# Optimization experiments

Measured on AMD Instinct MI355X. Metric: run time of the kernel, lower is better.

## Reference

```python
import jax, jax.numpy as jnp
import numpy as np

B, N, L = 32, 50, 16384  # batch, n_templates, segment length
KT = 4096                # template kernel length


def conv1d(x, w, pad, groups=1):
    # x: [B, Cin, L], w: [Cout, Cin/groups, K] (torch layout)
    return jax.lax.conv_general_dilated(
        x, w, window_strides=(1,), padding=[(pad, pad)],
        dimension_numbers=('NCH', 'OIH', 'NCH'), feature_group_count=groups)


def maxpool3(x):
    # MaxPool1d(kernel=3, stride=3), floor mode (VALID)
    return jax.lax.reduce_window(x, -jnp.inf, jax.lax.max,
                                 (1, 1, 3), (1, 1, 3), 'VALID')


def pad_to(x, m):
    p = (-x.shape[-1]) % m
    pads = ((0, 0),) * (x.ndim - 1) + ((0, p),)
    return jnp.pad(x, pads)


def setup_inputs() -> dict:
    key = jax.random.key(0)
    ks = jax.random.split(key, 12)
    return dict(
        xi=jax.random.normal(ks[0], (B, 2, L), jnp.float32),
        S_t_m12=jax.random.normal(ks[1], (2, 1, L), jnp.float32) * 0.01,
        template=jax.random.normal(ks[2], (N, 2, KT), jnp.float32) * 0.01,
        hh_sqrt=jax.random.uniform(ks[3], (N, 2), jnp.float32) + 0.5,
        W1=jax.random.normal(ks[4], (16, 2, 3), jnp.float32) * 0.1,
        b1=jnp.zeros((16,), jnp.float32),
        W2=jax.random.normal(ks[5], (32, 16, 3), jnp.float32) * 0.1,
        b2=jnp.zeros((32,), jnp.float32),
        W3=jax.random.normal(ks[6], (32, 128), jnp.float32) * 0.1,
        b3=jnp.zeros((32,), jnp.float32),
        W4=jax.random.normal(ks[7], (2, 32), jnp.float32) * 0.1,
        b4=jnp.zeros((2,), jnp.float32),
    )


def reference(xi, S_t_m12, template, hh_sqrt, W1, b1, W2, b2, W3, b3, W4, b4):
    # Whitening matched filter: grouped conv with kernel length L
    y = conv1d(xi, S_t_m12, L - 1, groups=2)          # [B, 2, 2L-1]
    y = pad_to(y, L)                                   # [B, 2, 2L]
    # wrap-fold each channel: reshape(B,2,L).sum over the fold axis
    d_SA = y[:, 0].reshape(-1, 2, L).sum(1)[:, None, :]  # [B,1,L]
    d_SE = y[:, 1].reshape(-1, 2, L).sum(1)[:, None, :]
    h_SA = template[:, 0, :].reshape(-1, 1, KT)          # [N,1,KT]
    h_SE = template[:, 1, :].reshape(-1, 1, KT)
    dh_A = pad_to(conv1d(d_SA, h_SA, KT - 1), L).reshape(-1, N, 2, L).sum(2)  # [B,N,L]
    dh_E = pad_to(conv1d(d_SE, h_SE, KT - 1), L).reshape(-1, N, 2, L).sum(2)
    z = jnp.stack((dh_A, dh_E), -1).transpose(0, 2, 1, 3)  # [B,L,N,2]
    z = z / hh_sqrt                                         # broadcast [N,2]
    z = z.max(axis=1).transpose(0, 2, 1)                    # [B,2,N]
    # small CNN + MLP head
    h = maxpool3(jax.nn.sigmoid(conv1d(z, W1, 0) + b1[None, :, None]))  # [B,16,16]
    h = maxpool3(jax.nn.sigmoid(conv1d(h, W2, 0) + b2[None, :, None]))  # [B,32,4]
    h = h.reshape(h.shape[0], -1)                                        # [B,128]
    h = jax.nn.relu(h @ W3.T + b3)
    return h @ W4.T + b4                                                 # [B,2]
```

## Files before the change

kernel.cpp:

```cpp
#include <hip/hip_runtime.h>
#include <math.h>

#define L_LEN 16384
#define M_LEN 8192
#define KT_LEN 4096
#define BB 32
#define NTPL 50
#define SPEC_STRIDE 8224
#define NSIG 166
#define NT 512
#define PI_F 3.14159265358979323846f

typedef float cf2 __attribute__((ext_vector_type(2)));

__device__ __forceinline__ cf2 cmul(cf2 a, cf2 b) {
    cf2 byx = __builtin_shufflevector(b, b, 1, 0);
    return (cf2){a.x, a.x} * b + (cf2){-a.y, a.y} * byx;
}
__device__ __forceinline__ cf2 cmulc(cf2 a, cf2 b) {
    return a * (cf2){b.x, b.x} + (cf2){a.y, -a.x} * (cf2){b.y, b.y};
}
template<int SIGN>
__device__ __forceinline__ cf2 rot90(cf2 z) {
    return (SIGN < 0) ? (cf2){z.y, -z.x} : (cf2){-z.y, z.x};
}
template<int SIGN>
__device__ __forceinline__ cf2 ldT(const cf2* __restrict__ T, int idx) {
    cf2 t = T[idx];
    if (SIGN > 0) t.y = -t.y;
    return t;
}

__device__ __forceinline__ int swz(int i) { return i ^ (((i >> 5) & 15) << 1); }

__device__ __forceinline__ int pos(int f) {
    return ((f & 15) << 9) | (((f >> 4) & 15) << 5) |
           (((f >> 8) & 15) << 1) | ((f >> 12) & 1);
}

template<int SIGN>
__device__ __forceinline__ void dft16(cf2 x[16]) {
    const float S = (SIGN < 0) ? -1.f : 1.f;
    const cf2 w1 = {0.9238795325112867f, S * 0.3826834323650898f};
    const cf2 w2 = {0.7071067811865476f, S * 0.7071067811865476f};
    const cf2 w3 = {0.3826834323650898f, S * 0.9238795325112867f};
    cf2 v[16];
    #pragma unroll
    for (int n1 = 0; n1 < 4; ++n1) {
        cf2 a0 = x[n1], a1 = x[n1+4], a2 = x[n1+8], a3 = x[n1+12];
        cf2 t0 = a0 + a2, t2 = a0 - a2;
        cf2 t1 = a1 + a3, t3 = rot90<SIGN>(a1 - a3);
        cf2 u0 = t0 + t1, u1 = t2 + t3;
        cf2 u2 = t0 - t1, u3 = t2 - t3;
        if (n1 == 1) { u1 = cmul(u1, w1); u2 = cmul(u2, w2); u3 = cmul(u3, w3); }
        else if (n1 == 2) { u1 = cmul(u1, w2); u2 = rot90<SIGN>(u2);
                            u3 = rot90<SIGN>(cmul(u3, w2)); }
        else if (n1 == 3) { u1 = cmul(u1, w3); u2 = rot90<SIGN>(cmul(u2, w2));
                            u3 = -cmul(u3, w1); }
        v[0*4+n1] = u0; v[1*4+n1] = u1; v[2*4+n1] = u2; v[3*4+n1] = u3;
    }
    #pragma unroll
    for (int r = 0; r < 4; ++r) {
        cf2 a0 = v[r*4+0], a1 = v[r*4+1], a2 = v[r*4+2], a3 = v[r*4+3];
        cf2 t0 = a0 + a2, t2 = a0 - a2;
        cf2 t1 = a1 + a3, t3 = rot90<SIGN>(a1 - a3);
        x[r]    = t0 + t1; x[r+4]  = t2 + t3;
        x[r+8]  = t0 - t1; x[r+12] = t2 - t3;
    }
}

template<int SIGN>
__device__ __forceinline__ void butterfly16(cf2* A, const int idx[16], cf2 w1) {
    cf2 x[16];
    #pragma unroll
    for (int n = 0; n < 16; ++n) x[n] = A[idx[n]];
    dft16<SIGN>(x);
    A[idx[0]] = x[0];
    A[idx[1]] = cmul(x[1], w1);
    const cf2 w2 = cmul(w1, w1);
    A[idx[2]] = cmul(x[2], w2);
    const cf2 w3 = cmul(w1, w2);
    A[idx[3]] = cmul(x[3], w3);
    const cf2 w4 = cmul(w2, w2);
    A[idx[4]] = cmul(x[4], w4);
    A[idx[5]] = cmul(x[5], cmul(w1, w4));
    A[idx[6]] = cmul(x[6], cmul(w2, w4));
    A[idx[7]] = cmul(x[7], cmul(w3, w4));
    const cf2 w8 = cmul(w4, w4);
    A[idx[8]]  = cmul(x[8],  w8);
    A[idx[9]]  = cmul(x[9],  cmul(w1, w8));
    A[idx[10]] = cmul(x[10], cmul(w2, w8));
    A[idx[11]] = cmul(x[11], cmul(w3, w8));
    const cf2 w12 = cmul(w4, w8);
    A[idx[12]] = cmul(x[12], w12);
    A[idx[13]] = cmul(x[13], cmul(w1, w12));
    A[idx[14]] = cmul(x[14], cmul(w2, w12));
    A[idx[15]] = cmul(x[15], cmul(w3, w12));
}

template<int SIGN, bool TBL>
__device__ __forceinline__ void fft_3stages(cf2* A, const cf2* __restrict__ T, int tid) {
    {
        int idx[16]; const int b0 = swz(tid);
        #pragma unroll
        for (int n = 0; n < 16; ++n) idx[n] = b0 + 512*n;
        cf2 w1;
        if (TBL) w1 = ldT<SIGN>(T, 2*tid);
        else { float sn, cs; __sincosf((float)SIGN * PI_F * (float)(2*tid) / 8192.f, &sn, &cs);
               w1 = (cf2){cs, sn}; }
        butterfly16<SIGN>(A, idx, w1);
    }
    __syncthreads();
    {
        const int blk = tid >> 5, j = tid & 31, jb = blk*512;
        int idx[16];
        #pragma unroll
        for (int n = 0; n < 16; ++n) idx[n] = jb + 32*n + (j ^ (2*n));
        cf2 w1;
        if (TBL) w1 = ldT<SIGN>(T, 32*j);
        else { float sn, cs; __sincosf((float)SIGN * PI_F * (float)(32*j) / 8192.f, &sn, &cs);
               w1 = (cf2){cs, sn}; }
        butterfly16<SIGN>(A, idx, w1);
    }
    __syncthreads();
    {
        const int blk = tid >> 1, j = tid & 1;
        const int xv = (blk & 15) << 1, b3 = blk*32 + j;
        int idx[16];
        #pragma unroll
        for (int n = 0; n < 16; ++n) idx[n] = b3 + ((2*n) ^ xv);
        cf2 w1;
        if (TBL) w1 = ldT<SIGN>(T, 512*j);
        else { float sn, cs; __sincosf((float)SIGN * PI_F * (float)(512*j) / 8192.f, &sn, &cs);
               w1 = (cf2){cs, sn}; }
        butterfly16<SIGN>(A, idx, w1);
    }
    __syncthreads();
}

__global__ __launch_bounds__(NT, 4)
void fwd_fft_kernel(const float* __restrict__ xi, const float* __restrict__ w,
                    const float* __restrict__ tmpl, cf2* __restrict__ Tw,
                    cf2* __restrict__ spec) {
    __shared__ __attribute__((aligned(16))) cf2 A[M_LEN];
    const int sig = blockIdx.x;
    const int tid = threadIdx.x;

    if (sig >= NSIG) {
        const int k = (sig - NSIG) * NT + tid;
        const double a = -M_PI * (double)k / 8192.0;
        Tw[k] = (cf2){(float)cos(a), (float)sin(a)};
        return;
    }

    const float* src;
    int nre;
    if (sig < 64)      { src = xi   + sig * L_LEN;         nre = L_LEN; }
    else if (sig < 66) { src = w    + (sig - 64) * L_LEN;  nre = L_LEN; }
    else               { src = tmpl + (sig - 66) * KT_LEN; nre = KT_LEN; }
    const int nc = nre >> 1;
    const float4* s4 = (const float4*)src;
    const int g0 = tid ^ ((tid >> 4) & 15);
    #pragma unroll
    for (int m = 0; m < 8; ++m) {
        const int u = 2*tid + 1024*m;
        float4 vv = (u < nc) ? s4[tid + 512*m] : make_float4(0.f, 0.f, 0.f, 0.f);
        ((float4*)A)[g0 + 512*m] = vv;
    }
    __syncthreads();

    fft_3stages<-1, false>(A, nullptr, tid);

    #pragma unroll
    for (int m = 0; m < 8; ++m) {
        float4 pq = ((float4*)A)[g0 + 512*m];
        ((float4*)A)[g0 + 512*m] = make_float4(pq.x + pq.z, pq.y + pq.w,
                                               pq.x - pq.z, pq.y - pq.w);
    }
    __syncthreads();

    cf2* out = spec + (size_t)sig * SPEC_STRIDE;
    #pragma unroll
    for (int m = 0; m < 16; ++m) {
        const int f = tid + 512*m;
        const int fb = (M_LEN - f) & (M_LEN - 1);
        cf2 Za = A[swz(pos(f))];
        cf2 Zb = A[swz(pos(fb))];
        cf2 E = (cf2){0.5f*(Za.x + Zb.x), 0.5f*(Za.y - Zb.y)};
        cf2 D = (cf2){Za.x - Zb.x, Za.y + Zb.y};
        cf2 O = (cf2){0.5f*D.y, -0.5f*D.x};
        float sn, cs;
        __sincosf(-PI_F * (float)f / 8192.f, &sn, &cs);
        cf2 TO = (cf2){cs*O.x - sn*O.y, cs*O.y + sn*O.x};
        out[f] = E + TO;
    }
    if (tid == 0) {
        cf2 Za = A[swz(0)];
        out[M_LEN] = (cf2){Za.x - Za.y, 0.f};
    }
}

__global__ __launch_bounds__(512)
void premul_kernel(const cf2* __restrict__ T, cf2* __restrict__ spec) {
    const int bc = blockIdx.x;
    const int tid = threadIdx.x;
    const int c = bc & 1;
    cf2* Xs = spec + (size_t)bc * SPEC_STRIDE;
    const cf2* Ws = spec + (size_t)(64 + c) * SPEC_STRIDE;
    const int r = tid & 3;
    for (int f = tid; f <= M_LEN; f += 512) {
        cf2 t = cmulc(Xs[f], Ws[f]);
        cf2 p = T[(2*f) & (L_LEN - 1)];
        cf2 s = cmulc(t, p);
        cf2 o;
        if (r == 0)      o = s;
        else if (r == 1) o = (cf2){s.y, -s.x};
        else if (r == 2) o = -s;
        else             o = (cf2){-s.y, s.x};
        Xs[f] = o;
    }
}

__global__ __launch_bounds__(NT, 4)
void inv_fft_kernel(const cf2* __restrict__ spec, const cf2* __restrict__ T,
                    const float* __restrict__ hh, float* __restrict__ zarr) {
    __shared__ __attribute__((aligned(16))) cf2 A[M_LEN];
    const int idx = blockIdx.x;
    const int c = idx & 1;
    const int n = (idx >> 1) % NTPL;
    const int b = idx / (2 * NTPL);
    const int tid = threadIdx.x;

    const cf2* Ds = spec + (size_t)(b*2 + c)      * SPEC_STRIDE;
    const cf2* Hs = spec + (size_t)(66 + n*2 + c) * SPEC_STRIDE;
    const float4* D4 = (const float4*)Ds;
    const float4* H4 = (const float4*)Hs;
    const float4* T4 = (const float4*)T;
    const int g0 = tid ^ ((tid >> 4) & 15);

    #pragma unroll
    for (int m = 0; m < 4; ++m) {
        const int u = 2*tid + 1024*m;
        float4 df = D4[tid + 512*m], hf = H4[tid + 512*m];
        cf2 Sa0 = cmulc((cf2){df.x, df.y}, (cf2){hf.x, hf.y});
        cf2 Sa1 = cmulc((cf2){df.z, df.w}, (cf2){hf.z, hf.w});
        cf2 Sb0 = cmulc(Ds[M_LEN - u],     Hs[M_LEN - u]);
        cf2 Sb1 = cmulc(Ds[M_LEN - 1 - u], Hs[M_LEN - 1 - u]);
        float4 tw = T4[tid + 512*m];
        float cs0 = tw.x, sn0 = -tw.y;
        float Ex0 = 0.5f*(Sa0.x + Sb0.x), Ey0 = 0.5f*(Sa0.y - Sb0.y);
        float Dx0 = Sa0.x - Sb0.x,        Dy0 = Sa0.y + Sb0.y;
        float Ox0 = 0.5f*(cs0*Dx0 - sn0*Dy0), Oy0 = 0.5f*(cs0*Dy0 + sn0*Dx0);
        float cs1 = tw.z, sn1 = -tw.w;
        float Ex1 = 0.5f*(Sa1.x + Sb1.x), Ey1 = 0.5f*(Sa1.y - Sb1.y);
        float Dx1 = Sa1.x - Sb1.x,        Dy1 = Sa1.y + Sb1.y;
        float Ox1 = 0.5f*(cs1*Dx1 - sn1*Dy1), Oy1 = 0.5f*(cs1*Dy1 + sn1*Dx1);
        ((float4*)A)[g0 + 512*m] = make_float4(Ex0 - Oy0, Ey0 + Ox0,
                                               Ex1 - Oy1, Ey1 + Ox1);
        if (u > 0) A[swz(M_LEN - u)] = (cf2){Ex0 + Oy0, Ox0 - Ey0};
        A[swz(M_LEN - 1 - u)] = (cf2){Ex1 + Oy1, Ox1 - Ey1};
    }
    if (tid == 0) {
        cf2 S = cmulc(Ds[4096], Hs[4096]);
        A[swz(4096)] = (cf2){S.x, -S.y};
    }
    __syncthreads();

    fft_3stages<+1, true>(A, T, tid);

    float mx = -INFINITY;
    #pragma unroll
    for (int m = 0; m < 8; ++m) {
        float4 pq = ((const float4*)A)[g0 + 512*m];
        mx = fmaxf(mx, fmaxf(fmaxf(pq.x + pq.z, pq.y + pq.w),
                             fmaxf(pq.x - pq.z, pq.y - pq.w)));
    }
    __syncthreads();
    for (int off = 32; off > 0; off >>= 1)
        mx = fmaxf(mx, __shfl_xor(mx, off));
    const int lane = tid & 63, wv = tid >> 6;
    float* redf = (float*)A;
    if (lane == 0) redf[wv] = mx;
    __syncthreads();
    if (tid == 0) {
        float mm = redf[0];
        for (int i = 1; i < NT/64; ++i) mm = fmaxf(mm, redf[i]);
        zarr[(b*2 + c)*NTPL + n] = mm / ((float)M_LEN * hh[n*2 + c]);
    }
}

__global__ __launch_bounds__(256)
void head_kernel(const float* __restrict__ zarr,
                 const float* __restrict__ W1, const float* __restrict__ b1,
                 const float* __restrict__ W2, const float* __restrict__ b2,
                 const float* __restrict__ W3, const float* __restrict__ b3,
                 const float* __restrict__ W4, const float* __restrict__ b4,
                 float* __restrict__ out) {
    __shared__ float zl[2][NTPL];
    __shared__ float s1[16][48];
    __shared__ float p1[16][16];
    __shared__ float s2[32][14];
    __shared__ float hflat[128];
    __shared__ float h1[32];
    const int b = blockIdx.x, tid = threadIdx.x;

    for (int i = tid; i < 2*NTPL; i += 256) zl[i/NTPL][i%NTPL] = zarr[b*2*NTPL + i];
    __syncthreads();
    for (int i = tid; i < 16*48; i += 256) {
        const int o = i / 48, t = i % 48;
        float acc = b1[o];
        #pragma unroll
        for (int cc = 0; cc < 2; ++cc)
            #pragma unroll
            for (int k = 0; k < 3; ++k)
                acc += zl[cc][t+k] * W1[o*6 + cc*3 + k];
        s1[o][t] = 1.f / (1.f + __expf(-acc));
    }
    __syncthreads();
    for (int i = tid; i < 16*16; i += 256) {
        const int o = i / 16, u = i % 16;
        p1[o][u] = fmaxf(fmaxf(s1[o][3*u], s1[o][3*u+1]), s1[o][3*u+2]);
    }
    __syncthreads();
    for (int i = tid; i < 32*14; i += 256) {
        const int o = i / 14, t = i % 14;
        float acc = b2[o];
        for (int cc = 0; cc < 16; ++cc)
            #pragma unroll
            for (int k = 0; k < 3; ++k)
                acc += p1[cc][t+k] * W2[o*48 + cc*3 + k];
        s2[o][t] = 1.f / (1.f + __expf(-acc));
    }
    __syncthreads();
    for (int i = tid; i < 128; i += 256) {
        const int o = i / 4, u = i % 4;
        hflat[i] = fmaxf(fmaxf(s2[o][3*u], s2[o][3*u+1]), s2[o][3*u+2]);
    }
    __syncthreads();
    if (tid < 32) {
        float acc = b3[tid];
        for (int j = 0; j < 128; ++j) acc += hflat[j] * W3[tid*128 + j];
        h1[tid] = fmaxf(acc, 0.f);
    }
    __syncthreads();
    if (tid < 2) {
        float acc = b4[tid];
        for (int j = 0; j < 32; ++j) acc += h1[j] * W4[tid*32 + j];
        out[b*2 + tid] = acc;
    }
}

extern "C" void kernel_launch(void* const* d_in, const int* in_sizes, int n_in,
                              void* d_out, int out_size, void* d_ws, size_t ws_size,
                              hipStream_t stream) {
    const float* xi   = (const float*)d_in[0];
    const float* Sw   = (const float*)d_in[1];
    const float* tmpl = (const float*)d_in[2];
    const float* hh   = (const float*)d_in[3];
    const float* W1   = (const float*)d_in[4];
    const float* b1   = (const float*)d_in[5];
    const float* W2   = (const float*)d_in[6];
    const float* b2   = (const float*)d_in[7];
    const float* W3   = (const float*)d_in[8];
    const float* b3   = (const float*)d_in[9];
    const float* W4   = (const float*)d_in[10];
    const float* b4   = (const float*)d_in[11];
    float* out = (float*)d_out;

    cf2* T16  = (cf2*)d_ws;
    cf2* spec = T16 + 16384;
    float* zarr = (float*)(spec + (size_t)NSIG * SPEC_STRIDE);

    fwd_fft_kernel<<<dim3(NSIG + 32), dim3(NT), 0, stream>>>(xi, Sw, tmpl, T16, spec);
    premul_kernel<<<dim3(64), dim3(512), 0, stream>>>(T16, spec);
    inv_fft_kernel<<<dim3(BB * NTPL * 2), dim3(NT), 0, stream>>>(spec, T16, hh, zarr);
    head_kernel<<<dim3(BB), dim3(256), 0, stream>>>(zarr, W1, b1, W2, b2, W3, b3, W4, b4, out);
}
```

Measured before the change: 162.8 us.

## Use padded LDS layout for FFT and fuse last inverse stage into max reduction

Replaces the XOR swizzle with a padding layout (one extra slot every 32 elements) and rewrites the three FFT stages as constant-stride butterflies over the padded shared array. In the inverse kernel, the final radix-16 stage and the radix-2 stage are now done in registers, with a lane-pair shuffle feeding the running max directly. This drops one LDS write/read pass and one barrier. In exchange, the padded layout costs a little extra shared memory and gives up vectorised float4 LDS accesses for scalar cf2 ones.

```diff
diff --git a/kernel.cpp b/kernel.cpp
--- a/kernel.cpp
+++ b/kernel.cpp
@@ -10,6 +10,8 @@
 #define NSIG 166
 #define NT 512
 #define PI_F 3.14159265358979323846f
+#define C16 0.98078528040323044f
+#define S16 0.19509032201612827f
 
 typedef float cf2 __attribute__((ext_vector_type(2)));
 
@@ -31,7 +33,7 @@
     return t;
 }
 
-__device__ __forceinline__ int swz(int i) { return i ^ (((i >> 5) & 15) << 1); }
+__device__ __forceinline__ int phys(int i) { return i + (i >> 5); }
 
 __device__ __forceinline__ int pos(int f) {
     return ((f & 15) << 9) | (((f >> 4) & 15) << 5) |
@@ -69,80 +71,40 @@
     }
 }
 
-template<int SIGN>
-__device__ __forceinline__ void butterfly16(cf2* A, const int idx[16], cf2 w1) {
+template<int SIGN, int OFS>
+__device__ __forceinline__ void butterfly16_lds(cf2* A, int base, cf2 w1) {
     cf2 x[16];
     #pragma unroll
-    for (int n = 0; n < 16; ++n) x[n] = A[idx[n]];
+    for (int n = 0; n < 16; ++n) x[n] = A[base + OFS*n];
     dft16<SIGN>(x);
-    A[idx[0]] = x[0];
-    A[idx[1]] = cmul(x[1], w1);
+    A[base] = x[0];
+    A[base + OFS] = cmul(x[1], w1);
     const cf2 w2 = cmul(w1, w1);
-    A[idx[2]] = cmul(x[2], w2);
+    A[base + OFS*2] = cmul(x[2], w2);
     const cf2 w3 = cmul(w1, w2);
-    A[idx[3]] = cmul(x[3], w3);
+    A[base + OFS*3] = cmul(x[3], w3);
     const cf2 w4 = cmul(w2, w2);
-    A[idx[4]] = cmul(x[4], w4);
-    A[idx[5]] = cmul(x[5], cmul(w1, w4));
-    A[idx[6]] = cmul(x[6], cmul(w2, w4));
-    A[idx[7]] = cmul(x[7], cmul(w3, w4));
+    A[base + OFS*4] = cmul(x[4], w4);
+    A[base + OFS*5] = cmul(x[5], cmul(w1, w4));
+    A[base + OFS*6] = cmul(x[6], cmul(w2, w4));
+    A[base + OFS*7] = cmul(x[7], cmul(w3, w4));
     const cf2 w8 = cmul(w4, w4);
-    A[idx[8]]  = cmul(x[8],  w8);
-    A[idx[9]]  = cmul(x[9],  cmul(w1, w8));
-    A[idx[10]] = cmul(x[10], cmul(w2, w8));
-    A[idx[11]] = cmul(x[11], cmul(w3, w8));
+    A[base + OFS*8]  = cmul(x[8],  w8);
+    A[base + OFS*9]  = cmul(x[9],  cmul(w1, w8));
+    A[base + OFS*10] = cmul(x[10], cmul(w2, w8));
+    A[base + OFS*11] = cmul(x[11], cmul(w3, w8));
     const cf2 w12 = cmul(w4, w8);
-    A[idx[12]] = cmul(x[12], w12);
-    A[idx[13]] = cmul(x[13], cmul(w1, w12));
-    A[idx[14]] = cmul(x[14], cmul(w2, w12));
-    A[idx[15]] = cmul(x[15], cmul(w3, w12));
-}
-
-template<int SIGN, bool TBL>
-__device__ __forceinline__ void fft_3stages(cf2* A, const cf2* __restrict__ T, int tid) {
-    {
-        int idx[16]; const int b0 = swz(tid);
-        #pragma unroll
-        for (int n = 0; n < 16; ++n) idx[n] = b0 + 512*n;
-        cf2 w1;
-        if (TBL) w1 = ldT<SIGN>(T, 2*tid);
-        else { float sn, cs; __sincosf((float)SIGN * PI_F * (float)(2*tid) / 8192.f, &sn, &cs);
-               w1 = (cf2){cs, sn}; }
-        butterfly16<SIGN>(A, idx, w1);
-    }
-    __syncthreads();
-    {
-        const int blk = tid >> 5, j = tid & 31, jb = blk*512;
-        int idx[16];
-        #pragma unroll
-        for (int n = 0; n < 16; ++n) idx[n] = jb + 32*n + (j ^ (2*n));
-        cf2 w1;
-        if (TBL) w1 = ldT<SIGN>(T, 32*j);
-        else { float sn, cs; __sincosf((float)SIGN * PI_F * (float)(32*j) / 8192.f, &sn, &cs);
-               w1 = (cf2){cs, sn}; }
-        butterfly16<SIGN>(A, idx, w1);
-    }
-    __syncthreads();
-    {
-        const int blk = tid >> 1, j = tid & 1;
-        const int xv = (blk & 15) << 1, b3 = blk*32 + j;
-        int idx[16];
-        #pragma unroll
-        for (int n = 0; n < 16; ++n) idx[n] = b3 + ((2*n) ^ xv);
-        cf2 w1;
-        if (TBL) w1 = ldT<SIGN>(T, 512*j);
-        else { float sn, cs; __sincosf((float)SIGN * PI_F * (float)(512*j) / 8192.f, &sn, &cs);
-               w1 = (cf2){cs, sn}; }
-        butterfly16<SIGN>(A, idx, w1);
-    }
-    __syncthreads();
+    A[base + OFS*12] = cmul(x[12], w12);
+    A[base + OFS*13] = cmul(x[13], cmul(w1, w12));
+    A[base + OFS*14] = cmul(x[14], cmul(w2, w12));
+    A[base + OFS*15] = cmul(x[15], cmul(w3, w12));
 }
 
 __global__ __launch_bounds__(NT, 4)
 void fwd_fft_kernel(const float* __restrict__ xi, const float* __restrict__ w,
                     const float* __restrict__ tmpl, cf2* __restrict__ Tw,
                     cf2* __restrict__ spec) {
-    __shared__ __attribute__((aligned(16))) cf2 A[M_LEN];
+    __shared__ __attribute__((aligned(16))) cf2 A[M_LEN + 256];
     const int sig = blockIdx.x;
     const int tid = threadIdx.x;
 
@@ -160,22 +122,38 @@
     else               { src = tmpl + (sig - 66) * KT_LEN; nre = KT_LEN; }
     const int nc = nre >> 1;
     const float4* s4 = (const float4*)src;
-    const int g0 = tid ^ ((tid >> 4) & 15);
     #pragma unroll
     for (int m = 0; m < 8; ++m) {
         const int u = 2*tid + 1024*m;
         float4 vv = (u < nc) ? s4[tid + 512*m] : make_float4(0.f, 0.f, 0.f, 0.f);
-        ((float4*)A)[g0 + 512*m] = vv;
-    }
-    __syncthreads();
-
-    fft_3stages<-1, false>(A, nullptr, tid);
-
+        const int p = phys(u);
+        A[p]   = (cf2){vv.x, vv.y};
+        A[p+1] = (cf2){vv.z, vv.w};
+    }
+    __syncthreads();
+
+    {
+        float sn, cs; __sincosf(-PI_F * (float)(2*tid) / 8192.f, &sn, &cs);
+        butterfly16_lds<-1, 528>(A, tid + (tid >> 5), (cf2){cs, sn});
+    }
+    __syncthreads();
+    {
+        const int blk = tid >> 5, j = tid & 31;
+        float sn, cs; __sincosf(-PI_F * (float)(32*j) / 8192.f, &sn, &cs);
+        butterfly16_lds<-1, 33>(A, 528*blk + j, (cf2){cs, sn});
+    }
+    __syncthreads();
+    {
+        const int blk = tid >> 1, j = tid & 1;
+        cf2 w1 = j ? (cf2){C16, -S16} : (cf2){1.f, 0.f};
+        butterfly16_lds<-1, 2>(A, 33*blk + j, w1);
+    }
+    __syncthreads();
     #pragma unroll
     for (int m = 0; m < 8; ++m) {
-        float4 pq = ((float4*)A)[g0 + 512*m];
-        ((float4*)A)[g0 + 512*m] = make_float4(pq.x + pq.z, pq.y + pq.w,
-                                               pq.x - pq.z, pq.y - pq.w);
+        const int p = phys(2*(tid + 512*m));
+        cf2 a = A[p], b = A[p+1];
+        A[p] = a + b; A[p+1] = a - b;
     }
     __syncthreads();
 
@@ -184,8 +162,8 @@
     for (int m = 0; m < 16; ++m) {
         const int f = tid + 512*m;
         const int fb = (M_LEN - f) & (M_LEN - 1);
-        cf2 Za = A[swz(pos(f))];
-        cf2 Zb = A[swz(pos(fb))];
+        cf2 Za = A[phys(pos(f))];
+        cf2 Zb = A[phys(pos(fb))];
         cf2 E = (cf2){0.5f*(Za.x + Zb.x), 0.5f*(Za.y - Zb.y)};
         cf2 D = (cf2){Za.x - Zb.x, Za.y + Zb.y};
         cf2 O = (cf2){0.5f*D.y, -0.5f*D.x};
@@ -195,7 +173,7 @@
         out[f] = E + TO;
     }
     if (tid == 0) {
-        cf2 Za = A[swz(0)];
+        cf2 Za = A[0];
         out[M_LEN] = (cf2){Za.x - Za.y, 0.f};
     }
 }
@@ -224,7 +202,7 @@
 __global__ __launch_bounds__(NT, 4)
 void inv_fft_kernel(const cf2* __restrict__ spec, const cf2* __restrict__ T,
                     const float* __restrict__ hh, float* __restrict__ zarr) {
-    __shared__ __attribute__((aligned(16))) cf2 A[M_LEN];
+    __shared__ __attribute__((aligned(16))) cf2 A[M_LEN + 256];
     const int idx = blockIdx.x;
     const int c = idx & 1;
     const int n = (idx >> 1) % NTPL;
@@ -236,7 +214,6 @@
     const float4* D4 = (const float4*)Ds;
     const float4* H4 = (const float4*)Hs;
     const float4* T4 = (const float4*)T;
-    const int g0 = tid ^ ((tid >> 4) & 15);
 
     #pragma unroll
     for (int m = 0; m < 4; ++m) {
@@ -255,29 +232,65 @@
         float Ex1 = 0.5f*(Sa1.x + Sb1.x), Ey1 = 0.5f*(Sa1.y - Sb1.y);
         float Dx1 = Sa1.x - Sb1.x,        Dy1 = Sa1.y + Sb1.y;
         float Ox1 = 0.5f*(cs1*Dx1 - sn1*Dy1), Oy1 = 0.5f*(cs1*Dy1 + sn1*Dx1);
-        ((float4*)A)[g0 + 512*m] = make_float4(Ex0 - Oy0, Ey0 + Ox0,
-                                               Ex1 - Oy1, Ey1 + Ox1);
-        if (u > 0) A[swz(M_LEN - u)] = (cf2){Ex0 + Oy0, Ox0 - Ey0};
-        A[swz(M_LEN - 1 - u)] = (cf2){Ex1 + Oy1, Ox1 - Ey1};
+        const int p = phys(u);
+        A[p]   = (cf2){Ex0 - Oy0, Ey0 + Ox0};
+        A[p+1] = (cf2){Ex1 - Oy1, Ey1 + Ox1};
+        if (u > 0) A[phys(M_LEN - u)] = (cf2){Ex0 + Oy0, Ox0 - Ey0};
+        A[phys(M_LEN - 1 - u)] = (cf2){Ex1 + Oy1, Ox1 - Ey1};
     }
     if (tid == 0) {
         cf2 S = cmulc(Ds[4096], Hs[4096]);
-        A[swz(4096)] = (cf2){S.x, -S.y};
-    }
-    __syncthreads();
-
-    fft_3stages<+1, true>(A, T, tid);
+        A[phys(4096)] = (cf2){S.x, -S.y};
+    }
+    __syncthreads();
+
+    butterfly16_lds<+1, 528>(A, tid + (tid >> 5), ldT<+1>(T, 2*tid));
+    __syncthreads();
+    { const int blk = tid >> 5, j = tid & 31;
+      butterfly16_lds<+1, 33>(A, 528*blk + j, ldT<+1>(T, 32*j)); }
+    __syncthreads();
 
     float mx = -INFINITY;
-    #pragma unroll
-    for (int m = 0; m < 8; ++m) {
-        float4 pq = ((const float4*)A)[g0 + 512*m];
-        mx = fmaxf(mx, fmaxf(fmaxf(pq.x + pq.z, pq.y + pq.w),
-                             fmaxf(pq.x - pq.z, pq.y - pq.w)));
-    }
-    __syncthreads();
+    {
+        const int blk = tid >> 1, j = tid & 1;
+        const int base3 = 33*blk + j;
+        cf2 x[16];
+        #pragma unroll
+        for (int nn = 0; nn < 16; ++nn) x[nn] = A[base3 + 2*nn];
+        dft16<+1>(x);
+        cf2 w1 = j ? (cf2){C16, S16} : (cf2){1.f, 0.f};
+        auto acc = [&](cf2 z) {
+            float qx = __shfl_xor(z.x, 1), qy = __shfl_xor(z.y, 1);
+            float sx = z.x + qx, sy = z.y + qy;
+            float dx = j ? qx - z.x : z.x - qx;
+            float dy = j ? qy - z.y : z.y - qy;
+            mx = fmaxf(mx, fmaxf(fmaxf(sx, sy), fmaxf(dx, dy)));
+        };
+        acc(x[0]);
+        acc(cmul(x[1], w1));
+        const cf2 w2 = cmul(w1, w1);
+        acc(cmul(x[2], w2));
+        const cf2 w3 = cmul(w1, w2);
+        acc(cmul(x[3], w3));
+        const cf2 w4 = cmul(w2, w2);
+        acc(cmul(x[4], w4));
+        acc(cmul(x[5], cmul(w1, w4)));
+        acc(cmul(x[6], cmul(w2, w4)));
+        acc(cmul(x[7], cmul(w3, w4)));
+        const cf2 w8 = cmul(w4, w4);
+        acc(cmul(x[8],  w8));
+        acc(cmul(x[9],  cmul(w1, w8)));
+        acc(cmul(x[10], cmul(w2, w8)));
+        acc(cmul(x[11], cmul(w3, w8)));
+        const cf2 w12 = cmul(w4, w8);
+        acc(cmul(x[12], w12));
+        acc(cmul(x[13], cmul(w1, w12)));
+        acc(cmul(x[14], cmul(w2, w12)));
+        acc(cmul(x[15], cmul(w3, w12)));
+    }
     for (int off = 32; off > 0; off >>= 1)
         mx = fmaxf(mx, __shfl_xor(mx, off));
+    __syncthreads();
     const int lane = tid & 63, wv = tid >> 6;
     float* redf = (float*)A;
     if (lane == 0) redf[wv] = mx;
```

Measured after the change: 164.9 us. No clear change (+1.3%).
